# Kernel optimization log

Hardware: AMD Instinct MI355X
Metric: run time of the kernel (lower is better)

## Reference

```python
import jax, jax.numpy as jnp
import numpy as np

B, N, C, H = 16, 207, 64, 64

def setup_inputs() -> dict:
    key = jax.random.key(0)
    k1, k2, k3, k4, k5 = jax.random.split(key, 5)
    return {
        "x": jax.random.normal(k1, (B, N, C), dtype=jnp.float32),
        "state": jax.random.normal(k2, (B, N, 1, H), dtype=jnp.float32),
        "Wx": jax.random.normal(k3, (B, N, C, 3 * H), dtype=jnp.float32) * 0.1,
        "Wh": jax.random.normal(k4, (B, N, H, 3 * H), dtype=jnp.float32) * 0.1,
        "b": jax.random.normal(k5, (B, N, 1, 3 * H), dtype=jnp.float32) * 0.1,
    }

def reference(x, state, Wx, Wh, b):
    # x: [B,N,C] -> [B,N,1,C]; state (h): [B,N,1,H]
    if x.ndim == 3:
        x = x[..., None, :]
    h = state
    dim_hidden = Wh.shape[-2]
    # One fused batched matmul for x @ Wx, then split into r/z/c parts.
    xW = jnp.matmul(x, Wx)  # [B,N,1,3H]
    xr, xz, xc = jnp.split(xW, 3, axis=-1)
    Wrh, Wzh, Wch = jnp.split(Wh, 3, axis=-1)
    br, bz, bc = jnp.split(b, 3, axis=-1)
    r = jax.nn.sigmoid(xr + jnp.matmul(h, Wrh) + br)
    z = jax.nn.sigmoid(xz + jnp.matmul(h, Wzh) + bz)
    # Note torch precedence: r * h @ Wch == (r * h) @ Wch
    hc = jnp.tanh(xc + jnp.matmul(r * h, Wch) + bc)
    h_new = (1.0 - z) * h + z * hc  # [B,N,1,H]
    return h_new
```

## Files before the change

kernel.cpp:

```cpp
#include <hip/hip_runtime.h>
#include <math.h>


#define GC 64
#define GH 64
#define J3 192
#define WPP (GC * J3)

__global__ __launch_bounds__(256, 8) void gru_cell_v3(
    const float* __restrict__ x,
    const float* __restrict__ state,
    const float* __restrict__ Wx,
    const float* __restrict__ Wh,
    const float* __restrict__ b,
    float* __restrict__ out)
{
    const int pos = blockIdx.x;
    const int t = threadIdx.x;

    __shared__ float x_s[GC];
    __shared__ float mult_s[2 * GH];
    __shared__ float part[1024];
    __shared__ float z_s[GH];

    if (t < GC)           x_s[t]          = x[(size_t)pos * GC + t];
    else if (t < GC + GH) mult_s[t - GC]  = state[(size_t)pos * GH + (t - GC)];
    __syncthreads();

    const float4* __restrict__ Wx4 = (const float4*)(Wx + (size_t)pos * WPP);
    const float4* __restrict__ Wh4 = (const float4*)(Wh + (size_t)pos * WPP);

    {
        const int jg = t & 15;
        const int rp = t >> 4;
        float4 acc = {0.f, 0.f, 0.f, 0.f};
        #pragma unroll
        for (int k = 0; k < 4; ++k) {
            const int c = rp + 16 * k;
            const float4 wx4 = Wx4[c * 48 + jg];
            const float4 wh4 = Wh4[c * 48 + jg];
            const float xs = x_s[c];
            const float hs = mult_s[c];
            acc.x += xs * wx4.x + hs * wh4.x;
            acc.y += xs * wx4.y + hs * wh4.y;
            acc.z += xs * wx4.z + hs * wh4.z;
            acc.w += xs * wx4.w + hs * wh4.w;
        }
        *((float4*)&part[rp * 64 + 4 * jg]) = acc;
    }
    __syncthreads();

    if (t < GH) {
        float v = b[(size_t)pos * J3 + t];
        #pragma unroll
        for (int rp = 0; rp < 16; ++rp) v += part[rp * 64 + t];
        const float r = 1.f / (1.f + expf(-v));
        mult_s[GH + t] = r * mult_s[t];
    }
    __syncthreads();

    float vc = 0.f;
    {
        const int jg = t & 31;
        const int rp = t >> 5;
        const int msel = (jg & 16) << 2;
        float4 acc = {0.f, 0.f, 0.f, 0.f};
        #pragma unroll 4
        for (int k = 0; k < 8; ++k) {
            const int c = rp + 8 * k;
            const float4 wx4 = Wx4[c * 48 + 16 + jg];
            const float4 wh4 = Wh4[c * 48 + 16 + jg];
            const float xs = x_s[c];
            const float ms = mult_s[msel + c];
            acc.x += xs * wx4.x + ms * wh4.x;
            acc.y += xs * wx4.y + ms * wh4.y;
            acc.z += xs * wx4.z + ms * wh4.z;
            acc.w += xs * wx4.w + ms * wh4.w;
        }
        *((float4*)&part[rp * 128 + 4 * jg]) = acc;
    }
    __syncthreads();

    if (t < 2 * GH) {
        float v = b[(size_t)pos * J3 + GH + t];
        #pragma unroll
        for (int rp = 0; rp < 8; ++rp) v += part[rp * 128 + t];
        if (t < GH) z_s[t] = 1.f / (1.f + expf(-v));
        else        vc = v;
    }
    __syncthreads();

    if (t >= GH && t < 2 * GH) {
        const int j = t - GH;
        const float hc = tanhf(vc);
        const float z = z_s[j];
        out[(size_t)pos * GH + j] = (1.f - z) * mult_s[j] + z * hc;
    }
}

extern "C" void kernel_launch(void* const* d_in, const int* in_sizes, int n_in,
                              void* d_out, int out_size, void* d_ws, size_t ws_size,
                              hipStream_t stream) {
    const float* x     = (const float*)d_in[0];
    const float* state = (const float*)d_in[1];
    const float* Wx    = (const float*)d_in[2];
    const float* Wh    = (const float*)d_in[3];
    const float* b     = (const float*)d_in[4];
    float* out = (float*)d_out;

    const int npos = in_sizes[0] / GC;

    gru_cell_v3<<<npos, 256, 0, stream>>>(x, state, Wx, Wh, b, out);
}
```

Measured before the change: 340.1 us.

## Prefetch all weight tiles into registers upfront and broadcast x/h via shuffles

All Wx/Wh float4 loads for both phases, plus the bias loads, are now issued at kernel start into registers. The phase-two weight fetch therefore no longer waits behind the first reduction and sigmoid barrier. The x/h shared-memory staging and its barrier are replaced by wavefront shuffles, and launch bounds drop from 8 to 4 blocks per SM to allow the larger register footprint. This raises memory-level parallelism in a bandwidth-bound kernel at the cost of occupancy.

```diff
diff --git a/kernel.cpp b/kernel.cpp
--- a/kernel.cpp
+++ b/kernel.cpp
@@ -7,7 +7,7 @@
 #define J3 192
 #define WPP (GC * J3)
 
-__global__ __launch_bounds__(256, 8) void gru_cell_v3(
+__global__ __launch_bounds__(256, 4) void gru_cell_v4(
     const float* __restrict__ x,
     const float* __restrict__ state,
     const float* __restrict__ Wx,
@@ -17,72 +17,85 @@
 {
     const int pos = blockIdx.x;
     const int t = threadIdx.x;
+    const int lane = t & 63;
 
-    __shared__ float x_s[GC];
     __shared__ float mult_s[2 * GH];
     __shared__ float part[1024];
     __shared__ float z_s[GH];
 
-    if (t < GC)           x_s[t]          = x[(size_t)pos * GC + t];
-    else if (t < GC + GH) mult_s[t - GC]  = state[(size_t)pos * GH + (t - GC)];
-    __syncthreads();
+    const float xv = x[(size_t)pos * GC + lane];
+    const float hv = state[(size_t)pos * GH + lane];
+    float bv1 = 0.f, bv2 = 0.f;
+    if (t < GH)     bv1 = b[(size_t)pos * J3 + t];
+    if (t < 2 * GH) bv2 = b[(size_t)pos * J3 + GH + t];
 
     const float4* __restrict__ Wx4 = (const float4*)(Wx + (size_t)pos * WPP);
     const float4* __restrict__ Wh4 = (const float4*)(Wh + (size_t)pos * WPP);
 
+    const int jg1 = t & 15, rp1 = t >> 4;
+    const int jg2 = t & 31, rp2 = t >> 5;
+
+    float4 wx1[4], wh1[4];
+    float4 wx2[8], wh2[8];
+    #pragma unroll
+    for (int k = 0; k < 4; ++k) {
+        const int c = rp1 + 16 * k;
+        wx1[k] = Wx4[c * 48 + jg1];
+        wh1[k] = Wh4[c * 48 + jg1];
+    }
+    #pragma unroll
+    for (int k = 0; k < 8; ++k) {
+        const int c = rp2 + 8 * k;
+        wx2[k] = Wx4[c * 48 + 16 + jg2];
+        wh2[k] = Wh4[c * 48 + 16 + jg2];
+    }
+
     {
-        const int jg = t & 15;
-        const int rp = t >> 4;
         float4 acc = {0.f, 0.f, 0.f, 0.f};
         #pragma unroll
         for (int k = 0; k < 4; ++k) {
-            const int c = rp + 16 * k;
-            const float4 wx4 = Wx4[c * 48 + jg];
-            const float4 wh4 = Wh4[c * 48 + jg];
-            const float xs = x_s[c];
-            const float hs = mult_s[c];
-            acc.x += xs * wx4.x + hs * wh4.x;
-            acc.y += xs * wx4.y + hs * wh4.y;
-            acc.z += xs * wx4.z + hs * wh4.z;
-            acc.w += xs * wx4.w + hs * wh4.w;
+            const int c = rp1 + 16 * k;
+            const float xs = __shfl(xv, c);
+            const float hs = __shfl(hv, c);
+            acc.x += xs * wx1[k].x + hs * wh1[k].x;
+            acc.y += xs * wx1[k].y + hs * wh1[k].y;
+            acc.z += xs * wx1[k].z + hs * wh1[k].z;
+            acc.w += xs * wx1[k].w + hs * wh1[k].w;
         }
-        *((float4*)&part[rp * 64 + 4 * jg]) = acc;
+        *((float4*)&part[rp1 * 64 + 4 * jg1]) = acc;
     }
     __syncthreads();
 
     if (t < GH) {
-        float v = b[(size_t)pos * J3 + t];
+        float v = bv1;
         #pragma unroll
         for (int rp = 0; rp < 16; ++rp) v += part[rp * 64 + t];
         const float r = 1.f / (1.f + expf(-v));
-        mult_s[GH + t] = r * mult_s[t];
+        mult_s[t]      = hv;
+        mult_s[GH + t] = r * hv;
+    }
+    __syncthreads();
+
+    {
+        const int msel = (jg2 & 16) << 2;
+        float4 acc = {0.f, 0.f, 0.f, 0.f};
+        #pragma unroll
+        for (int k = 0; k < 8; ++k) {
+            const int c = rp2 + 8 * k;
+            const float xs = __shfl(xv, c);
+            const float ms = mult_s[msel + c];
+            acc.x += xs * wx2[k].x + ms * wh2[k].x;
+            acc.y += xs * wx2[k].y + ms * wh2[k].y;
+            acc.z += xs * wx2[k].z + ms * wh2[k].z;
+            acc.w += xs * wx2[k].w + ms * wh2[k].w;
+        }
+        *((float4*)&part[rp2 * 128 + 4 * jg2]) = acc;
     }
     __syncthreads();
 
     float vc = 0.f;
-    {
-        const int jg = t & 31;
-        const int rp = t >> 5;
-        const int msel = (jg & 16) << 2;
-        float4 acc = {0.f, 0.f, 0.f, 0.f};
-        #pragma unroll 4
-        for (int k = 0; k < 8; ++k) {
-            const int c = rp + 8 * k;
-            const float4 wx4 = Wx4[c * 48 + 16 + jg];
-            const float4 wh4 = Wh4[c * 48 + 16 + jg];
-            const float xs = x_s[c];
-            const float ms = mult_s[msel + c];
-            acc.x += xs * wx4.x + ms * wh4.x;
-            acc.y += xs * wx4.y + ms * wh4.y;
-            acc.z += xs * wx4.z + ms * wh4.z;
-            acc.w += xs * wx4.w + ms * wh4.w;
-        }
-        *((float4*)&part[rp * 128 + 4 * jg]) = acc;
-    }
-    __syncthreads();
-
     if (t < 2 * GH) {
-        float v = b[(size_t)pos * J3 + GH + t];
+        float v = bv2;
         #pragma unroll
         for (int rp = 0; rp < 8; ++rp) v += part[rp * 128 + t];
         if (t < GH) z_s[t] = 1.f / (1.f + expf(-v));
@@ -110,5 +123,5 @@
 
     const int npos = in_sizes[0] / GC;
 
-    gru_cell_v3<<<npos, 256, 0, stream>>>(x, state, Wx, Wh, b, out);
+    gru_cell_v4<<<npos, 256, 0, stream>>>(x, state, Wx, Wh, b, out);
 }
```

After: 331.8 us. 1.03x faster.
